# Optimization experiments

Measured on AMD Instinct MI355X. Metric: run time of the kernel, lower is better.

## Reference

```python
import jax, jax.numpy as jnp
import numpy as np

EPS = 1e-3  # BN1d eps from norm_cfg


def _vfe_layer(x, W, gamma, beta, max_out, cat_max):
    """x: (N, M, Cin); W: (Cout, Cin) torch Linear layout; BN in training mode
    (batch stats over voxels N and points M per channel), then ReLU."""
    y = jnp.einsum('nmc,oc->nmo', x, W)            # (N, M, Cout)
    mean = y.mean(axis=(0, 1))                     # (Cout,)
    var = y.var(axis=(0, 1))                       # biased var, as BN uses
    y = (y - mean) * jax.lax.rsqrt(var + EPS) * gamma + beta
    pointwise = jax.nn.relu(y)                     # (N, M, Cout)
    if not max_out:
        return pointwise
    aggregated = pointwise.max(axis=1, keepdims=True)  # (N, 1, Cout)
    if not cat_max:
        return aggregated[:, 0, :]                 # (N, Cout)
    M = x.shape[1]
    repeated = jnp.broadcast_to(aggregated, (x.shape[0], M, aggregated.shape[2]))
    return jnp.concatenate([pointwise, repeated], axis=2)  # (N, M, 2*Cout)


def setup_inputs() -> dict:
    key = jax.random.key(0)
    ks = jax.random.split(key, 3)
    N, M, C = 20000, 64, 10
    return {
        'voxel_feats': jax.random.normal(ks[0], (N, M, C), dtype=jnp.float32),
        'W0': jax.random.normal(ks[1], (64, C), dtype=jnp.float32) * (1.0 / np.sqrt(C)),
        'gamma0': jnp.ones((64,), dtype=jnp.float32),
        'beta0': jnp.zeros((64,), dtype=jnp.float32),
        'W1': jax.random.normal(ks[2], (128, 128), dtype=jnp.float32) * (1.0 / np.sqrt(128)),
        'gamma1': jnp.ones((128,), dtype=jnp.float32),
        'beta1': jnp.zeros((128,), dtype=jnp.float32),
    }


def reference(voxel_feats, W0, gamma0, beta0, W1, gamma1, beta1):
    # layer 0: in=10 -> out=64, max_out=True, cat_max=True -> (N, M, 128)
    x = _vfe_layer(voxel_feats, W0, gamma0, beta0, max_out=True, cat_max=True)
    # layer 1 (last): in=128 -> out=128, max_out=True, cat_max=False -> (N, 128)
    x = _vfe_layer(x, W1, gamma1, beta1, max_out=True, cat_max=False)
    return x
```

## Files before the change

### kernel.cpp

```cpp
#include <hip/hip_runtime.h>

#define NVOX 20000
#define MPTS 64
#define CIN  10
#define NM   (NVOX*MPTS)
#define EPSBN 1e-3f

#define WS_SCALE0 0
#define WS_SHIFT0 64
#define WS_SCALE1 128
#define WS_SHIFT1 256

#define NB0   1024
#define P0STR 72
#define NBP   2000
#define NITER 5

typedef short bf16x8 __attribute__((ext_vector_type(8)));
typedef float f32x4  __attribute__((ext_vector_type(4)));
typedef unsigned int u32x4 __attribute__((ext_vector_type(4)));

__device__ __forceinline__ unsigned short f2bf(float f) {
    union { float f; unsigned u; } v; v.f = f;
    unsigned r = v.u + 0x7FFFu + ((v.u >> 16) & 1u);
    return (unsigned short)(r >> 16);
}
__device__ __forceinline__ unsigned cvtpk(float lo, float hi) {
    unsigned d;
    asm("v_cvt_pk_bf16_f32 %0, %1, %2" : "=v"(d) : "v"(lo), "v"(hi));
    return d;
}
__device__ __forceinline__ unsigned pkmax(unsigned a, unsigned b) {
    unsigned d;
    asm("v_pk_max_u16 %0, %1, %2" : "=v"(d) : "v"(a), "v"(b));
    return d;
}

__global__ __launch_bounds__(256) void k_stats0(const float* __restrict__ x,
                                                float* __restrict__ p0) {
    __shared__ float sm[4][P0STR];
    float sx[CIN];
    float sxx[55];
#pragma unroll
    for (int i = 0; i < CIN; i++) sx[i] = 0.f;
#pragma unroll
    for (int k = 0; k < 55; k++) sxx[k] = 0.f;

    const int t = threadIdx.x;
    const int tid = blockIdx.x * 256 + t;

    for (int g = tid; g < NM / 2; g += NB0 * 256) {
        const float4* xp = (const float4*)(x + (size_t)g * 20);
        float4 a = xp[0], b = xp[1], c = xp[2], d = xp[3], e = xp[4];
        float v0[CIN] = {a.x, a.y, a.z, a.w, b.x, b.y, b.z, b.w, c.x, c.y};
        float v1[CIN] = {c.z, c.w, d.x, d.y, d.z, d.w, e.x, e.y, e.z, e.w};
#pragma unroll
        for (int i = 0; i < CIN; i++) sx[i] += v0[i] + v1[i];
#pragma unroll
        for (int i = 0; i < CIN; i++)
#pragma unroll
            for (int j = 0; j <= i; j++)
                sxx[i * (i + 1) / 2 + j] += v0[i] * v0[j] + v1[i] * v1[j];
    }

    const int l = t & 63, w = t >> 6;
#pragma unroll
    for (int i = 0; i < CIN; i++) {
        float v = sx[i];
#pragma unroll
        for (int off = 32; off; off >>= 1) v += __shfl_xor(v, off, 64);
        if (l == 0) sm[w][i] = v;
    }
#pragma unroll
    for (int k = 0; k < 55; k++) {
        float v = sxx[k];
#pragma unroll
        for (int off = 32; off; off >>= 1) v += __shfl_xor(v, off, 64);
        if (l == 0) sm[w][10 + k] = v;
    }
    __syncthreads();
    if (t < 65)
        p0[blockIdx.x * P0STR + t] = sm[0][t] + sm[1][t] + sm[2][t] + sm[3][t];
}

__global__ void k_finalize0(const float* __restrict__ p0, float* __restrict__ ws,
                            const float* __restrict__ w0,
                            const float* __restrict__ gamma0, const float* __restrict__ beta0) {
    __shared__ float s[P0STR];
    const int t = threadIdx.x;
    if (t < 65) {
        float acc = 0.f;
#pragma unroll 8
        for (int r = 0; r < NB0; r++) acc += p0[r * P0STR + t];
        s[t] = acc;
    }
    __syncthreads();
    if (t < 64) {
        float w[CIN];
#pragma unroll
        for (int i = 0; i < CIN; i++) w[i] = w0[t * CIN + i];
        float m = 0.f;
#pragma unroll
        for (int i = 0; i < CIN; i++) m += w[i] * s[i];
        m *= (1.f / NM);
        float q = 0.f;
#pragma unroll
        for (int i = 0; i < CIN; i++)
#pragma unroll
            for (int j = 0; j <= i; j++)
                q += ((i == j) ? 1.f : 2.f) * w[i] * w[j] * s[10 + i * (i + 1) / 2 + j];
        q *= (1.f / NM);
        float var = q - m * m;
        float scale = gamma0[t] * rsqrtf(var + EPSBN);
        ws[WS_SCALE0 + t] = scale;
        ws[WS_SHIFT0 + t] = beta0[t] - m * scale;
    }
}

__global__ void k_finalize1(const float* __restrict__ p1, float* __restrict__ ws,
                            const float* __restrict__ gamma1, const float* __restrict__ beta1) {
    __shared__ float sm[2][4];
    const int c = blockIdx.x;
    const int t = threadIdx.x, l = t & 63, w = t >> 6;
    float s = 0.f, qq = 0.f;
    for (int r = t; r < NBP; r += 256) {
        s  += p1[(size_t)r * 256 + c];
        qq += p1[(size_t)r * 256 + 128 + c];
    }
#pragma unroll
    for (int off = 32; off; off >>= 1) { s += __shfl_xor(s, off, 64); qq += __shfl_xor(qq, off, 64); }
    if (l == 0) { sm[0][w] = s; sm[1][w] = qq; }
    __syncthreads();
    if (t == 0) {
        float S = sm[0][0] + sm[0][1] + sm[0][2] + sm[0][3];
        float Q = sm[1][0] + sm[1][1] + sm[1][2] + sm[1][3];
        float m = S * (1.f / NM);
        float var = Q * (1.f / NM) - m * m;
        float scale = gamma1[c] * rsqrtf(var + EPSBN);
        ws[WS_SCALE1 + c] = scale;
        ws[WS_SHIFT1 + c] = beta1[c] - m * scale;
    }
}

template <bool STATS>
__global__ __launch_bounds__(256) void k_pass(const float* __restrict__ x,
                                              const float* __restrict__ w0,
                                              const float* __restrict__ w1,
                                              const float* __restrict__ ws,
                                              float* __restrict__ pout) {
    __shared__ unsigned short zB[2][2][MPTS * 72];
    __shared__ unsigned short aggP[2][2][4 * 64];
    __shared__ float pbuf[256];

    const int t  = threadIdx.x;
    const int l  = t & 63;
    const int w  = t >> 6;
    const int lr = l & 15;
    const int lg = l >> 4;
    const int prow = 16 * w + lr;

    bf16x8 w0f[4];
#pragma unroll
    for (int mi = 0; mi < 4; mi++) {
        int ch = 16 * mi + lr;
        float sc = ws[WS_SCALE0 + ch], sh = ws[WS_SHIFT0 + ch];
        bf16x8 f;
#pragma unroll
        for (int j = 0; j < 8; j++) {
            int k = 8 * lg + j;
            float v = (k < CIN) ? sc * w0[ch * CIN + k] : (k == CIN ? sh : 0.f);
            f[j] = (short)f2bf(v);
        }
        w0f[mi] = f;
    }

    bf16x8 wfrag[2][4];
#pragma unroll
    for (int njl = 0; njl < 2; njl++) {
        const float* wrow = w1 + (32 * w + 16 * njl + lr) * 128;
#pragma unroll
        for (int ks = 0; ks < 4; ks++) {
            float4 a = *(const float4*)(wrow + 32 * ks + 8 * lg);
            float4 b = *(const float4*)(wrow + 32 * ks + 8 * lg + 4);
            bf16x8 f;
            f[0] = (short)f2bf(a.x); f[1] = (short)f2bf(a.y);
            f[2] = (short)f2bf(a.z); f[3] = (short)f2bf(a.w);
            f[4] = (short)f2bf(b.x); f[5] = (short)f2bf(b.y);
            f[6] = (short)f2bf(b.z); f[7] = (short)f2bf(b.w);
            wfrag[njl][ks] = f;
        }
    }

    float sc1[2], sh1[2];
    if (!STATS) {
#pragma unroll
        for (int njl = 0; njl < 2; njl++) {
            int col = 32 * w + 16 * njl + lr;
            sc1[njl] = ws[WS_SCALE1 + col];
            sh1[njl] = ws[WS_SHIFT1 + col];
        }
    }
    float as_[2] = {0.f, 0.f}, aq[2] = {0.f, 0.f};

    auto PF = [&](int n, float2& r0, float2& r1, float2& r2, float2& r3) {
        const float* xr = x + (size_t)n * 640 + prow * CIN;
        if (lg == 0) {
            r0 = *(const float2*)(xr + 0); r1 = *(const float2*)(xr + 2);
            r2 = *(const float2*)(xr + 4); r3 = *(const float2*)(xr + 6);
        } else if (lg == 1) {
            r0 = *(const float2*)(xr + 8);
        }
    };
    auto MKBX = [&](float2 r0, float2 r1, float2 r2, float2 r3) -> bf16x8 {
        u32x4 u = {0u, 0u, 0u, 0u};
        if (lg == 0) {
            u[0] = cvtpk(r0.x, r0.y); u[1] = cvtpk(r1.x, r1.y);
            u[2] = cvtpk(r2.x, r2.y); u[3] = cvtpk(r3.x, r3.y);
        } else if (lg == 1) {
            u[0] = cvtpk(r0.x, r0.y);
            u[1] = 0x00003F80u;
        }
        return __builtin_bit_cast(bf16x8, u);
    };
    auto L0 = [&](bf16x8 bx, int buf, int s) {
#pragma unroll
        for (int mi = 0; mi < 4; mi++) {
            f32x4 zz = {0.f, 0.f, 0.f, 0.f};
            f32x4 a0 = __builtin_amdgcn_mfma_f32_16x16x32_bf16(w0f[mi], bx, zz, 0, 0, 0);
            uint2 dd = { cvtpk(fmaxf(a0[0], 0.f), fmaxf(a0[1], 0.f)),
                         cvtpk(fmaxf(a0[2], 0.f), fmaxf(a0[3], 0.f)) };
            *(uint2*)&zB[buf][s][prow * 72 + 16 * mi + 4 * lg] = dd;
        }
    };
    auto AGG = [&](int buf, int s) {
        int cs = l & 7;
        int pa = 16 * w + 2 * (l >> 3);
        u32x4 ra = *(const u32x4*)&zB[buf][s][pa * 72 + cs * 8];
        u32x4 rb = *(const u32x4*)&zB[buf][s][(pa + 1) * 72 + cs * 8];
        u32x4 m;
#pragma unroll
        for (int k2 = 0; k2 < 4; k2++) m[k2] = pkmax(ra[k2], rb[k2]);
#pragma unroll
        for (int off = 8; off <= 32; off <<= 1)
#pragma unroll
            for (int k2 = 0; k2 < 4; k2++) m[k2] = pkmax(m[k2], __shfl_xor(m[k2], off));
        if (l < 8) *(u32x4*)&aggP[buf][s][w * 64 + l * 8] = m;
    };
    auto CONSUME = [&](int buf, int s, int n) {
        bf16x8 bz[4][2];
#pragma unroll
        for (int pj = 0; pj < 4; pj++)
#pragma unroll
            for (int ks = 0; ks < 2; ks++)
                bz[pj][ks] = *(const bf16x8*)&zB[buf][s][(16 * pj + lr) * 72 + (4 * ks + lg) * 8];
        bf16x8 gf[2];
#pragma unroll
        for (int ks = 0; ks < 2; ks++) {
            int sl = (4 * ks + lg) * 8;
            u32x4 g = *(const u32x4*)&aggP[buf][s][sl];
#pragma unroll
            for (int wv = 1; wv < 4; wv++) {
                u32x4 h2 = *(const u32x4*)&aggP[buf][s][wv * 64 + sl];
#pragma unroll
                for (int k2 = 0; k2 < 4; k2++) g[k2] = pkmax(g[k2], h2[k2]);
            }
            gf[ks] = __builtin_bit_cast(bf16x8, g);
        }
        f32x4 dacc[2];
#pragma unroll
        for (int njl = 0; njl < 2; njl++) {
            f32x4 zz = {0.f, 0.f, 0.f, 0.f};
            zz = __builtin_amdgcn_mfma_f32_16x16x32_bf16(gf[0], wfrag[njl][2], zz, 0, 0, 0);
            dacc[njl] = __builtin_amdgcn_mfma_f32_16x16x32_bf16(gf[1], wfrag[njl][3], zz, 0, 0, 0);
        }
#pragma unroll
        for (int njl = 0; njl < 2; njl++) {
            float vm = 0.f;
#pragma unroll
            for (int mi = 0; mi < 4; mi++) {
                f32x4 acc = dacc[njl];
                acc = __builtin_amdgcn_mfma_f32_16x16x32_bf16(bz[mi][0], wfrag[njl][0], acc, 0, 0, 0);
                acc = __builtin_amdgcn_mfma_f32_16x16x32_bf16(bz[mi][1], wfrag[njl][1], acc, 0, 0, 0);
                if (STATS) {
#pragma unroll
                    for (int r = 0; r < 4; r++) { as_[njl] += acc[r]; aq[njl] += acc[r] * acc[r]; }
                } else {
#pragma unroll
                    for (int r = 0; r < 4; r++)
                        vm = fmaxf(vm, fmaxf(fmaf(acc[r], sc1[njl], sh1[njl]), 0.f));
                }
            }
            if (!STATS) {
                vm = fmaxf(vm, __shfl_xor(vm, 16));
                vm = fmaxf(vm, __shfl_xor(vm, 32));
                if (l < 16) pout[(size_t)n * 128 + 32 * w + 16 * njl + l] = vm;
            }
        }
    };

    float2 aA0, aA1, aA2, aA3, aB0, aB1, aB2, aB3;
    PF(blockIdx.x, aA0, aA1, aA2, aA3);
    PF(blockIdx.x + NBP, aB0, aB1, aB2, aB3);

    for (int k = 0; k < NITER; k++) {
        const int buf = k & 1;
        const int nA = blockIdx.x + k * 2 * NBP;
        const int nB = nA + NBP;

        bf16x8 bxA = MKBX(aA0, aA1, aA2, aA3);
        bf16x8 bxB = MKBX(aB0, aB1, aB2, aB3);
        if (k < NITER - 1) {
            PF(nA + 2 * NBP, aA0, aA1, aA2, aA3);
            PF(nB + 2 * NBP, aB0, aB1, aB2, aB3);
        }

        L0(bxA, buf, 0);
        L0(bxB, buf, 1);
        AGG(buf, 0);
        AGG(buf, 1);

        asm volatile("s_waitcnt lgkmcnt(0)" ::: "memory");
        __builtin_amdgcn_s_barrier();

        CONSUME(buf, 0, nA);
        CONSUME(buf, 1, nB);
    }

    if (STATS) {
#pragma unroll
        for (int njl = 0; njl < 2; njl++) {
            float s = as_[njl];
            s += __shfl_xor(s, 16); s += __shfl_xor(s, 32);
            float qq = aq[njl];
            qq += __shfl_xor(qq, 16); qq += __shfl_xor(qq, 32);
            if (l < 16) {
                int col = 32 * w + 16 * njl + l;
                pbuf[col] = s;
                pbuf[128 + col] = qq;
            }
        }
        __syncthreads();
        pout[(size_t)blockIdx.x * 256 + t] = pbuf[t];
    }
}

extern "C" void kernel_launch(void* const* d_in, const int* in_sizes, int n_in,
                              void* d_out, int out_size, void* d_ws, size_t ws_size,
                              hipStream_t stream) {
    (void)in_sizes; (void)n_in; (void)out_size; (void)ws_size;
    const float* x      = (const float*)d_in[0];
    const float* W0     = (const float*)d_in[1];
    const float* gamma0 = (const float*)d_in[2];
    const float* beta0  = (const float*)d_in[3];
    const float* W1     = (const float*)d_in[4];
    const float* gamma1 = (const float*)d_in[5];
    const float* beta1  = (const float*)d_in[6];
    float* out = (float*)d_out;
    float* ws  = (float*)d_ws;

    k_stats0<<<NB0, 256, 0, stream>>>(x, out);
    k_finalize0<<<1, 256, 0, stream>>>(out, ws, W0, gamma0, beta0);
    k_pass<true><<<NBP, 256, 0, stream>>>(x, W0, W1, ws, out);
    k_finalize1<<<128, 256, 0, stream>>>(out, ws, gamma1, beta1);
    k_pass<false><<<NBP, 256, 0, stream>>>(x, W0, W1, ws, out);
}
```

Baseline: 250.1 us.

## Software-pipeline one voxel per iteration and fold BN1 scale into weights

Restructures the per-block loop from processing two voxels per iteration into a one-voxel software pipeline. Layer-0 production for voxel k+1 overlaps consumption of voxel k in a double-buffered LDS slot, with two hard barriers per iteration. This halves the LDS footprint and raises the grid to 2500 blocks of 8 iterations. It also folds the layer-1 BN scale into the bf16 weight fragments and the shift into the MFMA accumulator init, which removes per-element FMAs. The trade-off is more barriers per voxel and a small precision change from scaling before bf16 rounding.

```diff
diff --git a/kernel.cpp b/kernel.cpp
--- a/kernel.cpp
+++ b/kernel.cpp
@@ -13,8 +13,8 @@
 
 #define NB0   1024
 #define P0STR 72
-#define NBP   2000
-#define NITER 5
+#define NBP   2500
+#define NITER 8
 
 typedef short bf16x8 __attribute__((ext_vector_type(8)));
 typedef float f32x4  __attribute__((ext_vector_type(4)));
@@ -35,6 +35,14 @@
     asm("v_pk_max_u16 %0, %1, %2" : "=v"(d) : "v"(a), "v"(b));
     return d;
 }
+
+#define HARD_BARRIER()                                        \
+    do {                                                      \
+        asm volatile("s_waitcnt lgkmcnt(0)" ::: "memory");    \
+        __builtin_amdgcn_sched_barrier(0);                    \
+        __builtin_amdgcn_s_barrier();                         \
+        __builtin_amdgcn_sched_barrier(0);                    \
+    } while (0)
 
 __global__ __launch_bounds__(256) void k_stats0(const float* __restrict__ x,
                                                 float* __restrict__ p0) {
@@ -148,8 +156,8 @@
                                               const float* __restrict__ w1,
                                               const float* __restrict__ ws,
                                               float* __restrict__ pout) {
-    __shared__ unsigned short zB[2][2][MPTS * 72];
-    __shared__ unsigned short aggP[2][2][4 * 64];
+    __shared__ unsigned short zB[2][MPTS * 72];
+    __shared__ unsigned short aggP[2][4 * 64];
     __shared__ float pbuf[256];
 
     const int t  = threadIdx.x;
@@ -174,69 +182,68 @@
         w0f[mi] = f;
     }
 
+    float sh1[2];
     bf16x8 wfrag[2][4];
 #pragma unroll
     for (int njl = 0; njl < 2; njl++) {
-        const float* wrow = w1 + (32 * w + 16 * njl + lr) * 128;
+        int col = 32 * w + 16 * njl + lr;
+        float scl = 1.f;
+        if constexpr (!STATS) {
+            scl = ws[WS_SCALE1 + col];
+            sh1[njl] = ws[WS_SHIFT1 + col];
+        } else {
+            sh1[njl] = 0.f;
+        }
+        const float* wrow = w1 + col * 128;
 #pragma unroll
         for (int ks = 0; ks < 4; ks++) {
             float4 a = *(const float4*)(wrow + 32 * ks + 8 * lg);
             float4 b = *(const float4*)(wrow + 32 * ks + 8 * lg + 4);
             bf16x8 f;
-            f[0] = (short)f2bf(a.x); f[1] = (short)f2bf(a.y);
-            f[2] = (short)f2bf(a.z); f[3] = (short)f2bf(a.w);
-            f[4] = (short)f2bf(b.x); f[5] = (short)f2bf(b.y);
-            f[6] = (short)f2bf(b.z); f[7] = (short)f2bf(b.w);
+            f[0] = (short)f2bf(scl * a.x); f[1] = (short)f2bf(scl * a.y);
+            f[2] = (short)f2bf(scl * a.z); f[3] = (short)f2bf(scl * a.w);
+            f[4] = (short)f2bf(scl * b.x); f[5] = (short)f2bf(scl * b.y);
+            f[6] = (short)f2bf(scl * b.z); f[7] = (short)f2bf(scl * b.w);
             wfrag[njl][ks] = f;
         }
     }
 
-    float sc1[2], sh1[2];
-    if (!STATS) {
-#pragma unroll
-        for (int njl = 0; njl < 2; njl++) {
-            int col = 32 * w + 16 * njl + lr;
-            sc1[njl] = ws[WS_SCALE1 + col];
-            sh1[njl] = ws[WS_SHIFT1 + col];
-        }
-    }
     float as_[2] = {0.f, 0.f}, aq[2] = {0.f, 0.f};
 
-    auto PF = [&](int n, float2& r0, float2& r1, float2& r2, float2& r3) {
+    float2 pfA, pfB, pfC, pfD;
+    auto PF = [&](int n) {
         const float* xr = x + (size_t)n * 640 + prow * CIN;
         if (lg == 0) {
-            r0 = *(const float2*)(xr + 0); r1 = *(const float2*)(xr + 2);
-            r2 = *(const float2*)(xr + 4); r3 = *(const float2*)(xr + 6);
+            pfA = *(const float2*)(xr + 0); pfB = *(const float2*)(xr + 2);
+            pfC = *(const float2*)(xr + 4); pfD = *(const float2*)(xr + 6);
         } else if (lg == 1) {
-            r0 = *(const float2*)(xr + 8);
+            pfA = *(const float2*)(xr + 8);
         }
     };
-    auto MKBX = [&](float2 r0, float2 r1, float2 r2, float2 r3) -> bf16x8 {
+    auto MKBX = [&]() -> bf16x8 {
         u32x4 u = {0u, 0u, 0u, 0u};
         if (lg == 0) {
-            u[0] = cvtpk(r0.x, r0.y); u[1] = cvtpk(r1.x, r1.y);
-            u[2] = cvtpk(r2.x, r2.y); u[3] = cvtpk(r3.x, r3.y);
+            u[0] = cvtpk(pfA.x, pfA.y); u[1] = cvtpk(pfB.x, pfB.y);
+            u[2] = cvtpk(pfC.x, pfC.y); u[3] = cvtpk(pfD.x, pfD.y);
         } else if (lg == 1) {
-            u[0] = cvtpk(r0.x, r0.y);
+            u[0] = cvtpk(pfA.x, pfA.y);
             u[1] = 0x00003F80u;
         }
         return __builtin_bit_cast(bf16x8, u);
     };
-    auto L0 = [&](bf16x8 bx, int buf, int s) {
+    auto PRODUCE = [&](bf16x8 bx, int buf) {
 #pragma unroll
         for (int mi = 0; mi < 4; mi++) {
             f32x4 zz = {0.f, 0.f, 0.f, 0.f};
             f32x4 a0 = __builtin_amdgcn_mfma_f32_16x16x32_bf16(w0f[mi], bx, zz, 0, 0, 0);
             uint2 dd = { cvtpk(fmaxf(a0[0], 0.f), fmaxf(a0[1], 0.f)),
                          cvtpk(fmaxf(a0[2], 0.f), fmaxf(a0[3], 0.f)) };
-            *(uint2*)&zB[buf][s][prow * 72 + 16 * mi + 4 * lg] = dd;
-        }
-    };
-    auto AGG = [&](int buf, int s) {
+            *(uint2*)&zB[buf][prow * 72 + 16 * mi + 4 * lg] = dd;
+        }
         int cs = l & 7;
         int pa = 16 * w + 2 * (l >> 3);
-        u32x4 ra = *(const u32x4*)&zB[buf][s][pa * 72 + cs * 8];
-        u32x4 rb = *(const u32x4*)&zB[buf][s][(pa + 1) * 72 + cs * 8];
+        u32x4 ra = *(const u32x4*)&zB[buf][pa * 72 + cs * 8];
+        u32x4 rb = *(const u32x4*)&zB[buf][(pa + 1) * 72 + cs * 8];
         u32x4 m;
 #pragma unroll
         for (int k2 = 0; k2 < 4; k2++) m[k2] = pkmax(ra[k2], rb[k2]);
@@ -244,32 +251,57 @@
         for (int off = 8; off <= 32; off <<= 1)
 #pragma unroll
             for (int k2 = 0; k2 < 4; k2++) m[k2] = pkmax(m[k2], __shfl_xor(m[k2], off));
-        if (l < 8) *(u32x4*)&aggP[buf][s][w * 64 + l * 8] = m;
+        if (l < 8) *(u32x4*)&aggP[buf][w * 64 + l * 8] = m;
     };
-    auto CONSUME = [&](int buf, int s, int n) {
+
+    PF(blockIdx.x);
+    bf16x8 bx0 = MKBX();
+    PF(blockIdx.x + NBP);
+    PRODUCE(bx0, 0);
+
+    for (int k = 0; k < NITER; k++) {
+        const int buf = k & 1;
+        const int n = blockIdx.x + k * NBP;
+
+        if (k < NITER - 1) {
+            bf16x8 bx = MKBX();
+            if (k < NITER - 2) PF(blockIdx.x + (k + 2) * NBP);
+            PRODUCE(bx, buf ^ 1);
+        }
+
+        HARD_BARRIER();
+
         bf16x8 bz[4][2];
 #pragma unroll
         for (int pj = 0; pj < 4; pj++)
 #pragma unroll
             for (int ks = 0; ks < 2; ks++)
-                bz[pj][ks] = *(const bf16x8*)&zB[buf][s][(16 * pj + lr) * 72 + (4 * ks + lg) * 8];
-        bf16x8 gf[2];
+                bz[pj][ks] = *(const bf16x8*)&zB[buf][(16 * pj + lr) * 72 + (4 * ks + lg) * 8];
+        u32x4 gp[2][4];
 #pragma unroll
         for (int ks = 0; ks < 2; ks++) {
             int sl = (4 * ks + lg) * 8;
-            u32x4 g = *(const u32x4*)&aggP[buf][s][sl];
-#pragma unroll
-            for (int wv = 1; wv < 4; wv++) {
-                u32x4 h2 = *(const u32x4*)&aggP[buf][s][wv * 64 + sl];
-#pragma unroll
-                for (int k2 = 0; k2 < 4; k2++) g[k2] = pkmax(g[k2], h2[k2]);
-            }
+#pragma unroll
+            for (int wv = 0; wv < 4; wv++)
+                gp[ks][wv] = *(const u32x4*)&aggP[buf][wv * 64 + sl];
+        }
+
+        HARD_BARRIER();
+
+        bf16x8 gf[2];
+#pragma unroll
+        for (int ks = 0; ks < 2; ks++) {
+            u32x4 g = gp[ks][0];
+#pragma unroll
+            for (int wv = 1; wv < 4; wv++)
+#pragma unroll
+                for (int k2 = 0; k2 < 4; k2++) g[k2] = pkmax(g[k2], gp[ks][wv][k2]);
             gf[ks] = __builtin_bit_cast(bf16x8, g);
         }
         f32x4 dacc[2];
 #pragma unroll
         for (int njl = 0; njl < 2; njl++) {
-            f32x4 zz = {0.f, 0.f, 0.f, 0.f};
+            f32x4 zz = {sh1[njl], sh1[njl], sh1[njl], sh1[njl]};
             zz = __builtin_amdgcn_mfma_f32_16x16x32_bf16(gf[0], wfrag[njl][2], zz, 0, 0, 0);
             dacc[njl] = __builtin_amdgcn_mfma_f32_16x16x32_bf16(gf[1], wfrag[njl][3], zz, 0, 0, 0);
         }
@@ -286,8 +318,7 @@
                     for (int r = 0; r < 4; r++) { as_[njl] += acc[r]; aq[njl] += acc[r] * acc[r]; }
                 } else {
 #pragma unroll
-                    for (int r = 0; r < 4; r++)
-                        vm = fmaxf(vm, fmaxf(fmaf(acc[r], sc1[njl], sh1[njl]), 0.f));
+                    for (int r = 0; r < 4; r++) vm = fmaxf(vm, fmaxf(acc[r], 0.f));
                 }
             }
             if (!STATS) {
@@ -296,34 +327,6 @@
                 if (l < 16) pout[(size_t)n * 128 + 32 * w + 16 * njl + l] = vm;
             }
         }
-    };
-
-    float2 aA0, aA1, aA2, aA3, aB0, aB1, aB2, aB3;
-    PF(blockIdx.x, aA0, aA1, aA2, aA3);
-    PF(blockIdx.x + NBP, aB0, aB1, aB2, aB3);
-
-    for (int k = 0; k < NITER; k++) {
-        const int buf = k & 1;
-        const int nA = blockIdx.x + k * 2 * NBP;
-        const int nB = nA + NBP;
-
-        bf16x8 bxA = MKBX(aA0, aA1, aA2, aA3);
-        bf16x8 bxB = MKBX(aB0, aB1, aB2, aB3);
-        if (k < NITER - 1) {
-            PF(nA + 2 * NBP, aA0, aA1, aA2, aA3);
-            PF(nB + 2 * NBP, aB0, aB1, aB2, aB3);
-        }
-
-        L0(bxA, buf, 0);
-        L0(bxB, buf, 1);
-        AGG(buf, 0);
-        AGG(buf, 1);
-
-        asm volatile("s_waitcnt lgkmcnt(0)" ::: "memory");
-        __builtin_amdgcn_s_barrier();
-
-        CONSUME(buf, 0, nA);
-        CONSUME(buf, 1, nB);
     }
 
     if (STATS) {
```

Result: slower. 291.1 us (+16.4%).
